# Kernel optimization log

Measured on AMD Instinct MI355X. Metric: run time of the kernel, lower is better.

Reference implementation:

```python
import jax, jax.numpy as jnp
import numpy as np

B, T, O = 8, 8, 25
C, H, W = 3, 192, 640
P = 16            # pooled output size / patch size
D = 768           # embed dim
GH, GW = 12, 2    # max adaptive sampling grid: ceil(H/P), ceil(2*r_max/P)


def setup_inputs() -> dict:
    key = jax.random.key(0)
    k1, k2, k3, k4, k5, k6 = jax.random.split(key, 6)
    features = jax.random.normal(k1, (B, C, T, H, W), jnp.float32)
    # keypoints (x, y, r); x >= H so that the source's buggy y2=min(x+r,H) still yields valid boxes
    kx = jax.random.uniform(k2, (B, T, O), minval=float(H), maxval=float(W))
    ky = jax.random.uniform(k3, (B, T, O), minval=0.0, maxval=float(H))
    kr = jax.random.uniform(k4, (B, T, O), minval=4.0, maxval=16.0)
    keypoints = jnp.stack([kx, ky, kr], axis=-1)
    conv_w = jax.random.normal(k5, (D, C, P, P), jnp.float32) * (1.0 / np.sqrt(C * P * P))
    conv_b = jax.random.normal(k6, (D,), jnp.float32) * 0.01
    return {"features": features, "keypoints": keypoints, "conv_w": conv_w, "conv_b": conv_b}


def _sample_coords(start, bin_sz, grid, G, size):
    # start,bin_sz,grid: [N]; returns coords y/x [N,P,G], validity mask, low idx, high idx, lerp weight
    N = start.shape[0]
    pb = jnp.arange(P, dtype=start.dtype)
    ig = jnp.arange(G, dtype=start.dtype)
    gf = jnp.maximum(grid, 1).astype(start.dtype)
    c = (start[:, None, None]
         + pb[None, :, None] * bin_sz[:, None, None]
         + (ig[None, None, :] + 0.5) * (bin_sz / gf)[:, None, None])  # [N,P,G]
    valid = (jnp.arange(G)[None, None, :] < grid[:, None, None]) & (c >= -1.0) & (c <= float(size))
    cc = jnp.clip(c, 0.0, float(size - 1))
    lo = jnp.floor(cc).astype(jnp.int32)
    hi = jnp.minimum(lo + 1, size - 1)
    l = cc - lo.astype(cc.dtype)  # fractional part (ly/lx)
    return valid, lo, hi, l


def _roi_align(feats_hw, boxes, img_idx):
    # feats_hw: [BT,H,W,C]; boxes: [N,4] xyxy; torchvision roi_align, aligned=True, sampling_ratio=-1
    x1, y1, x2, y2 = boxes[:, 0], boxes[:, 1], boxes[:, 2], boxes[:, 3]
    start_h, start_w = y1 - 0.5, x1 - 0.5  # aligned offset (spatial_scale=1)
    roi_h, roi_w = y2 - y1, x2 - x1        # aligned=True: no clamp to >=1
    bin_h, bin_w = roi_h / P, roi_w / P
    gh = jnp.ceil(roi_h / P).astype(jnp.int32)
    gw = jnp.ceil(roi_w / P).astype(jnp.int32)
    count = jnp.maximum(gh * gw, 1).astype(feats_hw.dtype)

    vy, y0, y1i, ly = _sample_coords(start_h, bin_h, gh, GH, H)  # [N,P,GH]
    vx, x0, x1i, lx = _sample_coords(start_w, bin_w, gw, GW, W)  # [N,P,GW]
    hy, hx = 1.0 - ly, 1.0 - lx

    def gather(yi, xi):  # -> [N,Ph,Pw,GH,GW,C]
        return feats_hw[img_idx[:, None, None, None, None],
                        yi[:, :, None, :, None],
                        xi[:, None, :, None, :]]

    w00 = hy[:, :, None, :, None] * hx[:, None, :, None, :]
    w01 = hy[:, :, None, :, None] * lx[:, None, :, None, :]
    w10 = ly[:, :, None, :, None] * hx[:, None, :, None, :]
    w11 = ly[:, :, None, :, None] * lx[:, None, :, None, :]
    val = (w00[..., None] * gather(y0, x0) + w01[..., None] * gather(y0, x1i)
           + w10[..., None] * gather(y1i, x0) + w11[..., None] * gather(y1i, x1i))
    mask = (vy[:, :, None, :, None] & vx[:, None, :, None, :])[..., None]
    val = jnp.where(mask, val, 0.0)
    return val.sum(axis=(3, 4)) / count[:, None, None, None]  # [N,P,P,C]


def _forward(features, keypoints, conv_w, conv_b):
    feats_hw = features.transpose(0, 2, 3, 4, 1).reshape(B * T, H, W, C)  # (b t) h w c
    kpts = keypoints.reshape(B * T * O, 3)
    kx, ky, kr = kpts[:, 0], kpts[:, 1], kpts[:, 2]
    # faithful to source (note: y2 uses x, a bug in the original module)
    bx1 = jnp.maximum(kx - kr, 0.0)
    by1 = jnp.maximum(ky - kr, 0.0)
    bx2 = jnp.minimum(kx + kr, float(W))
    by2 = jnp.minimum(kx + kr, float(H))
    boxes = jnp.stack([bx1, by1, bx2, by2], axis=-1)
    img_idx = jnp.arange(B * T * O, dtype=jnp.int32) // O
    pooled = _roi_align(feats_hw, boxes, img_idx)  # [N,P,P,C]
    # PxP conv with no padding on PxP input == flatten + linear
    out = jnp.einsum('nijc,dcij->nd', pooled, conv_w) + conv_b
    return out.reshape(B, T, O, D)


def reference(features, keypoints, conv_w, conv_b):
    return _forward(features, keypoints, conv_w, conv_b)
```

## Files before the change

### kernel.cpp

```cpp
#include <hip/hip_runtime.h>

#define NB 8
#define NT 8
#define NO 25
#define NC 3
#define NH 192
#define NW 640
#define NP 16
#define ND 768
#define NGH 12
#define NGW 2
#define NKP (NB*NT*NO)
#define NK (NC*NP*NP)
#define NTASK (NKP*NC)
#define NCVW ((NK*ND)/(256*4))

#define S_STRIDE 41

typedef __attribute__((ext_vector_type(4))) float  f32x4;
typedef __attribute__((ext_vector_type(8))) short  bf16x8;

static __device__ __forceinline__ unsigned short f2bf(float f) {
  union { float f; unsigned u; } x; x.f = f;
  unsigned r = x.u + 0x7FFFu + ((x.u >> 16) & 1u);
  return (unsigned short)(r >> 16);
}

__global__ __launch_bounds__(256) void pool_convw_kernel(
    const float* __restrict__ features,
    const float* __restrict__ keypoints,
    const float* __restrict__ conv_w,
    unsigned short* __restrict__ pooled,
    unsigned short* __restrict__ wbf)
{
  __shared__ float S[NH * S_STRIDE];

  const int bid = blockIdx.x;
  const int tid = threadIdx.x;

  if (bid < NCVW) {
    const int i = bid * 256 + tid;
    const float4 v = reinterpret_cast<const float4*>(conv_w)[i];
    ushort4 o;
    o.x = f2bf(v.x); o.y = f2bf(v.y); o.z = f2bf(v.z); o.w = f2bf(v.w);
    reinterpret_cast<ushort4*>(wbf)[i] = o;
    return;
  }

  const int rb = bid - NCVW;
  const int t  = (rb & 7) * (NTASK / 8) + (rb >> 3);
  const int n  = t / 3;
  const int ch = t - 3 * n;

  const float kx = keypoints[n * 3 + 0];
  const float ky = keypoints[n * 3 + 1];
  const float kr = keypoints[n * 3 + 2];

  const float bx1 = fmaxf(kx - kr, 0.0f);
  const float by1 = fmaxf(ky - kr, 0.0f);
  const float bx2 = fminf(kx + kr, (float)NW);
  const float by2 = fminf(kx + kr, (float)NH);

  const float start_h = by1 - 0.5f;
  const float start_w = bx1 - 0.5f;
  const float bin_h = (by2 - by1) * (1.0f / (float)NP);
  const float bin_w = (bx2 - bx1) * (1.0f / (float)NP);
  const int gh = (int)ceilf(bin_h);
  const int gw = (int)ceilf(bin_w);
  const float ghf = (float)max(gh, 1);
  const float gwf = (float)max(gw, 1);
  const float inv_count = 1.0f / (float)max(gh * gw, 1);
  const float sub_h = bin_h / ghf;
  const float sub_w = bin_w / gwf;

  const float cy_min = start_h + 0.5f * sub_h;
  const float cy_max = start_h + 15.0f * bin_h + ((float)(gh - 1) + 0.5f) * sub_h;
  const float cx_min = start_w + 0.5f * sub_w;
  const float cx_max = start_w + 15.0f * bin_w + ((float)(gw - 1) + 0.5f) * sub_w;
  const int rmin = (int)floorf(fminf(fmaxf(cy_min, 0.0f), (float)(NH - 1)));
  const int rmax = min((int)floorf(fminf(fmaxf(cy_max, 0.0f), (float)(NH - 1))) + 1, NH - 1);
  const int cmin = (int)floorf(fminf(fmaxf(cx_min, 0.0f), (float)(NW - 1)));
  const int cmax = min((int)floorf(fminf(fmaxf(cx_max, 0.0f), (float)(NW - 1))) + 1, NW - 1);
  const int nrows = rmax - rmin + 1;
  const int cmin_al = cmin & ~3;
  const int nq = ((cmax - cmin_al) >> 2) + 1;
  const int tot = nrows * nq;
  const float inv_nq = 1.0f / (float)nq;

  const int img  = n / NO;
  const int bb   = img / NT;
  const int timg = img % NT;
  const float* __restrict__ src =
      features + (size_t)((bb * NC + ch) * NT + timg) * (NH * NW);

  float4 v0, v1, v2, v3, v4, v5, v6, v7;
  int ro0, ro1, ro2, ro3, ro4, ro5, ro6, ro7;

#define STAGE_LOAD(Q, V, RO)                                                 \
  {                                                                          \
    const int e = tid + (Q << 8);                                            \
    if (e < tot) {                                                           \
      const int r  = (int)(((float)e + 0.5f) * inv_nq);                      \
      const int c4 = (e - r * nq) << 2;                                      \
      const int gc = cmin_al + c4;                                           \
      const float* p = src + (size_t)(rmin + r) * NW + gc;                   \
      if (gc + 3 < NW) { V = *reinterpret_cast<const float4*>(p); }          \
      else { V.x = p[0]; V.y = p[min(1, NW - 1 - gc)];                       \
             V.z = p[min(2, NW - 1 - gc)]; V.w = p[min(3, NW - 1 - gc)]; }   \
      RO = r * S_STRIDE + c4;                                                \
    } else { RO = -1; }                                                      \
  }

  STAGE_LOAD(0, v0, ro0) STAGE_LOAD(1, v1, ro1) STAGE_LOAD(2, v2, ro2)
  STAGE_LOAD(3, v3, ro3) STAGE_LOAD(4, v4, ro4) STAGE_LOAD(5, v5, ro5)
  STAGE_LOAD(6, v6, ro6) STAGE_LOAD(7, v7, ro7)
#undef STAGE_LOAD

#define STAGE_WRITE(V, RO)                                                   \
  if (RO >= 0) { float* s = &S[RO];                                          \
    s[0] = V.x; s[1] = V.y; s[2] = V.z; s[3] = V.w; }

  STAGE_WRITE(v0, ro0) STAGE_WRITE(v1, ro1) STAGE_WRITE(v2, ro2)
  STAGE_WRITE(v3, ro3) STAGE_WRITE(v4, ro4) STAGE_WRITE(v5, ro5)
  STAGE_WRITE(v6, ro6) STAGE_WRITE(v7, ro7)
#undef STAGE_WRITE

  const int padc = nq << 2;
  if (tid < nrows) S[tid * S_STRIDE + padc] = 0.0f;

  __syncthreads();

  const int i = tid >> 4;
  const int j = tid & 15;

  float lxv[NGW]; int cxv[NGW];
#pragma unroll
  for (int gx = 0; gx < NGW; ++gx) {
    const float c = start_w + (float)j * bin_w + ((float)gx + 0.5f) * sub_w;
    const float cc = fminf(fmaxf(c, 0.0f), (float)(NW - 1));
    const int x0 = (int)floorf(cc);
    lxv[gx] = cc - (float)x0;
    cxv[gx] = x0 - cmin_al;
  }

  float acc = 0.0f;
#pragma unroll
  for (int gy = 0; gy < NGH; ++gy) {
    if (gy >= gh) break;
    const float c = start_h + (float)i * bin_h + ((float)gy + 0.5f) * sub_h;
    const float cc = fminf(fmaxf(c, 0.0f), (float)(NH - 1));
    const int y0 = (int)floorf(cc);
    const float ly = cc - (float)y0;
    const float hy = 1.0f - ly;
    const int ry0 = (y0 - rmin) * S_STRIDE;
    const int ry1 = (min(y0 + 1, NH - 1) - rmin) * S_STRIDE;
#pragma unroll
    for (int gx = 0; gx < NGW; ++gx) {
      if (gx >= gw) break;
      const float lx = lxv[gx];
      const float hx = 1.0f - lx;
      const float* r0 = &S[ry0 + cxv[gx]];
      const float* r1 = &S[ry1 + cxv[gx]];
      const float v00 = r0[0], v01 = r0[1];
      const float v10 = r1[0], v11 = r1[1];
      acc += hy * (hx * v00 + lx * v01) + ly * (hx * v10 + lx * v11);
    }
  }
  pooled[(size_t)n * NK + ch * (NP * NP) + tid] = f2bf(acc * inv_count);
}

#define BM 64
#define BN 64
#define BK 64

static __device__ __forceinline__ void gld_lds16(const unsigned short* g,
                                                 unsigned short* l) {
  __builtin_amdgcn_global_load_lds(
      (const __attribute__((address_space(1))) unsigned int*)g,
      (__attribute__((address_space(3))) unsigned int*)l,
      16, 0, 0);
}

__global__ __launch_bounds__(256) void gemm_kernel(
    const unsigned short* __restrict__ A,
    const unsigned short* __restrict__ Bw,
    const float* __restrict__ bias,
    float* __restrict__ outp)
{
  __shared__ __align__(16) unsigned short As[2][BM * BK];
  __shared__ __align__(16) unsigned short Bs[2][BM * BK];

  const int tid = threadIdx.x;
  const int w = tid >> 6;
  const int l = tid & 63;
  const int bm = blockIdx.x * BM;
  const int bn = blockIdx.y * BN;

  const int wr = w >> 1, wc = w & 1;
  const int lr = l & 15;
  const int kh = l >> 4;

  const int rA0 = (wr << 5) + lr;
  const int rB0 = (wc << 5) + lr;

#define STAGE(buf, kk)                                                       \
  {                                                                          \
    _Pragma("unroll")                                                        \
    for (int q = 0; q < 2; ++q) {                                            \
      const int s   = (q << 8) + tid;                                        \
      const int row = s >> 3;                                                \
      const int c16 = (s & 7) ^ (row & 7);                                   \
      gld_lds16(A  + (size_t)(bm + row) * NK + (kk) + (c16 << 3),            \
                &As[buf][s << 3]);                                           \
      gld_lds16(Bw + (size_t)(bn + row) * NK + (kk) + (c16 << 3),            \
                &Bs[buf][s << 3]);                                           \
    }                                                                        \
  }

  f32x4 acc[2][2] = {};

  STAGE(0, 0)
  __syncthreads();

  int cur = 0;
  for (int it = 0; it < NK / BK; ++it) {
    if (it + 1 < NK / BK) STAGE(cur ^ 1, (it + 1) * BK)

#pragma unroll
    for (int ks = 0; ks < 2; ++ks) {
      const int kq = (ks << 2) + kh;
      const bf16x8 a0 = *reinterpret_cast<const bf16x8*>(
          &As[cur][(rA0 << 6) + ((kq ^ (rA0 & 7)) << 3)]);
      const bf16x8 a1 = *reinterpret_cast<const bf16x8*>(
          &As[cur][((rA0 + 16) << 6) + ((kq ^ (rA0 & 7)) << 3)]);
      const bf16x8 b0 = *reinterpret_cast<const bf16x8*>(
          &Bs[cur][(rB0 << 6) + ((kq ^ (rB0 & 7)) << 3)]);
      const bf16x8 b1 = *reinterpret_cast<const bf16x8*>(
          &Bs[cur][((rB0 + 16) << 6) + ((kq ^ (rB0 & 7)) << 3)]);
      acc[0][0] = __builtin_amdgcn_mfma_f32_16x16x32_bf16(a0, b0, acc[0][0], 0, 0, 0);
      acc[0][1] = __builtin_amdgcn_mfma_f32_16x16x32_bf16(a0, b1, acc[0][1], 0, 0, 0);
      acc[1][0] = __builtin_amdgcn_mfma_f32_16x16x32_bf16(a1, b0, acc[1][0], 0, 0, 0);
      acc[1][1] = __builtin_amdgcn_mfma_f32_16x16x32_bf16(a1, b1, acc[1][1], 0, 0, 0);
    }

    __syncthreads();
    cur ^= 1;
  }
#undef STAGE

#pragma unroll
  for (int ni = 0; ni < 2; ++ni) {
    const int col = bn + (wc << 5) + (ni << 4) + lr;
    const float bv = bias[col];
#pragma unroll
    for (int mi = 0; mi < 2; ++mi) {
      const int rbase = bm + (wr << 5) + (mi << 4) + (kh << 2);
#pragma unroll
      for (int q = 0; q < 4; ++q) {
        outp[(size_t)(rbase + q) * ND + col] = acc[mi][ni][q] + bv;
      }
    }
  }
}

extern "C" void kernel_launch(void* const* d_in, const int* in_sizes, int n_in,
                              void* d_out, int out_size, void* d_ws, size_t ws_size,
                              hipStream_t stream) {
  (void)in_sizes; (void)n_in; (void)out_size; (void)ws_size;
  const float* features  = (const float*)d_in[0];
  const float* keypoints = (const float*)d_in[1];
  const float* conv_w    = (const float*)d_in[2];
  const float* conv_b    = (const float*)d_in[3];
  float* outp = (float*)d_out;

  unsigned short* pooled = (unsigned short*)d_ws;
  unsigned short* wbf    = (unsigned short*)((char*)d_ws + 2457600);

  pool_convw_kernel<<<NCVW + NTASK, 256, 0, stream>>>(features, keypoints,
                                                      conv_w, pooled, wbf);

  dim3 grid(NKP / BM, ND / BN);
  gemm_kernel<<<grid, 256, 0, stream>>>(pooled, wbf, conv_b, outp);
}
```

Measured before the change: 38.48 us.

## Make pooling kernel persistent with register-prefetched next ROI task

Replaces one-block-per-(ROI,channel) pooling with a fixed grid of 672 persistent blocks, each looping over tasks assigned per XCD. While one task is computed from LDS, the next task's global loads are issued into registers, so load latency overlaps with compute. The conv weight bf16 conversion is spread across the same blocks instead of using separate blocks. This cuts block launch overhead and hides memory latency, at the cost of an extra sync per task, higher register pressure and possible load imbalance across blocks.

```diff
diff --git a/kernel.cpp b/kernel.cpp
--- a/kernel.cpp
+++ b/kernel.cpp
@@ -13,9 +13,14 @@
 #define NKP (NB*NT*NO)
 #define NK (NC*NP*NP)
 #define NTASK (NKP*NC)
-#define NCVW ((NK*ND)/(256*4))
 
 #define S_STRIDE 41
+
+#define POOL_BLOCKS 672
+#define TASKS_PER_XCD 600
+#define BLOCKS_PER_XCD 84
+#define CVW_TOTAL ((NK*ND)/4)
+#define CVW_PER_BLOCK 220
 
 typedef __attribute__((ext_vector_type(4))) float  f32x4;
 typedef __attribute__((ext_vector_type(8))) short  bf16x8;
@@ -26,7 +31,58 @@
   return (unsigned short)(r >> 16);
 }
 
-__global__ __launch_bounds__(256) void pool_convw_kernel(
+struct TaskGeom {
+  const float* src;
+  float start_h, start_w, bin_h, bin_w, sub_h, sub_w, inv_count, inv_nq;
+  int n, ch, gh, gw, rmin, cmin_al, nq, nrows, tot;
+};
+
+static __device__ __forceinline__ TaskGeom make_geom(
+    const float* __restrict__ features, const float* __restrict__ keypoints,
+    int t) {
+  TaskGeom G;
+  G.n  = t / 3;
+  G.ch = t - 3 * G.n;
+  const float kx = keypoints[G.n * 3 + 0];
+  const float ky = keypoints[G.n * 3 + 1];
+  const float kr = keypoints[G.n * 3 + 2];
+  const float bx1 = fmaxf(kx - kr, 0.0f);
+  const float by1 = fmaxf(ky - kr, 0.0f);
+  const float bx2 = fminf(kx + kr, (float)NW);
+  const float by2 = fminf(kx + kr, (float)NH);
+  G.start_h = by1 - 0.5f;
+  G.start_w = bx1 - 0.5f;
+  G.bin_h = (by2 - by1) * (1.0f / (float)NP);
+  G.bin_w = (bx2 - bx1) * (1.0f / (float)NP);
+  G.gh = (int)ceilf(G.bin_h);
+  G.gw = (int)ceilf(G.bin_w);
+  const float ghf = (float)max(G.gh, 1);
+  const float gwf = (float)max(G.gw, 1);
+  G.inv_count = 1.0f / (float)max(G.gh * G.gw, 1);
+  G.sub_h = G.bin_h / ghf;
+  G.sub_w = G.bin_w / gwf;
+  const float cy_min = G.start_h + 0.5f * G.sub_h;
+  const float cy_max = G.start_h + 15.0f * G.bin_h + ((float)(G.gh - 1) + 0.5f) * G.sub_h;
+  const float cx_min = G.start_w + 0.5f * G.sub_w;
+  const float cx_max = G.start_w + 15.0f * G.bin_w + ((float)(G.gw - 1) + 0.5f) * G.sub_w;
+  G.rmin = (int)floorf(fminf(fmaxf(cy_min, 0.0f), (float)(NH - 1)));
+  const int rmax = min((int)floorf(fminf(fmaxf(cy_max, 0.0f), (float)(NH - 1))) + 1, NH - 1);
+  const int cmin = (int)floorf(fminf(fmaxf(cx_min, 0.0f), (float)(NW - 1)));
+  const int cmax = min((int)floorf(fminf(fmaxf(cx_max, 0.0f), (float)(NW - 1))) + 1, NW - 1);
+  G.nrows = rmax - G.rmin + 1;
+  G.cmin_al = cmin & ~3;
+  G.nq = ((cmax - G.cmin_al) >> 2) + 1;
+  G.tot = G.nrows * G.nq;
+  G.inv_nq = 1.0f / (float)G.nq;
+  const int img  = G.n / NO;
+  const int bb   = img / NT;
+  const int timg = img - bb * NT;
+  G.src = features + (size_t)((bb * NC + G.ch) * NT + timg) * (NH * NW)
+        + (size_t)G.rmin * NW;
+  return G;
+}
+
+__global__ __launch_bounds__(256) void pool_kernel(
     const float* __restrict__ features,
     const float* __restrict__ keypoints,
     const float* __restrict__ conv_w,
@@ -35,138 +91,116 @@
 {
   __shared__ float S[NH * S_STRIDE];
 
-  const int bid = blockIdx.x;
+  const int p   = blockIdx.x;
   const int tid = threadIdx.x;
 
-  if (bid < NCVW) {
-    const int i = bid * 256 + tid;
-    const float4 v = reinterpret_cast<const float4*>(conv_w)[i];
-    ushort4 o;
-    o.x = f2bf(v.x); o.y = f2bf(v.y); o.z = f2bf(v.z); o.w = f2bf(v.w);
-    reinterpret_cast<ushort4*>(wbf)[i] = o;
-    return;
-  }
-
-  const int rb = bid - NCVW;
-  const int t  = (rb & 7) * (NTASK / 8) + (rb >> 3);
-  const int n  = t / 3;
-  const int ch = t - 3 * n;
-
-  const float kx = keypoints[n * 3 + 0];
-  const float ky = keypoints[n * 3 + 1];
-  const float kr = keypoints[n * 3 + 2];
-
-  const float bx1 = fmaxf(kx - kr, 0.0f);
-  const float by1 = fmaxf(ky - kr, 0.0f);
-  const float bx2 = fminf(kx + kr, (float)NW);
-  const float by2 = fminf(kx + kr, (float)NH);
-
-  const float start_h = by1 - 0.5f;
-  const float start_w = bx1 - 0.5f;
-  const float bin_h = (by2 - by1) * (1.0f / (float)NP);
-  const float bin_w = (bx2 - bx1) * (1.0f / (float)NP);
-  const int gh = (int)ceilf(bin_h);
-  const int gw = (int)ceilf(bin_w);
-  const float ghf = (float)max(gh, 1);
-  const float gwf = (float)max(gw, 1);
-  const float inv_count = 1.0f / (float)max(gh * gw, 1);
-  const float sub_h = bin_h / ghf;
-  const float sub_w = bin_w / gwf;
-
-  const float cy_min = start_h + 0.5f * sub_h;
-  const float cy_max = start_h + 15.0f * bin_h + ((float)(gh - 1) + 0.5f) * sub_h;
-  const float cx_min = start_w + 0.5f * sub_w;
-  const float cx_max = start_w + 15.0f * bin_w + ((float)(gw - 1) + 0.5f) * sub_w;
-  const int rmin = (int)floorf(fminf(fmaxf(cy_min, 0.0f), (float)(NH - 1)));
-  const int rmax = min((int)floorf(fminf(fmaxf(cy_max, 0.0f), (float)(NH - 1))) + 1, NH - 1);
-  const int cmin = (int)floorf(fminf(fmaxf(cx_min, 0.0f), (float)(NW - 1)));
-  const int cmax = min((int)floorf(fminf(fmaxf(cx_max, 0.0f), (float)(NW - 1))) + 1, NW - 1);
-  const int nrows = rmax - rmin + 1;
-  const int cmin_al = cmin & ~3;
-  const int nq = ((cmax - cmin_al) >> 2) + 1;
-  const int tot = nrows * nq;
-  const float inv_nq = 1.0f / (float)nq;
-
-  const int img  = n / NO;
-  const int bb   = img / NT;
-  const int timg = img % NT;
-  const float* __restrict__ src =
-      features + (size_t)((bb * NC + ch) * NT + timg) * (NH * NW);
+  const int widx = p * CVW_PER_BLOCK + tid;
+  const bool wact = (tid < CVW_PER_BLOCK) && (widx < CVW_TOTAL);
+  float4 wv = {};
+  if (wact) wv = reinterpret_cast<const float4*>(conv_w)[widx];
+
+  const int xcd = p & 7;
+  const int lb  = p >> 3;
+  const int tbase = xcd * TASKS_PER_XCD + lb;
+  const int ntasks = (TASKS_PER_XCD - lb + BLOCKS_PER_XCD - 1) / BLOCKS_PER_XCD;
+
+  TaskGeom gc = make_geom(features, keypoints, tbase);
 
   float4 v0, v1, v2, v3, v4, v5, v6, v7;
   int ro0, ro1, ro2, ro3, ro4, ro5, ro6, ro7;
 
-#define STAGE_LOAD(Q, V, RO)                                                 \
+#define STAGE_LOAD(G, Q, V, RO)                                              \
   {                                                                          \
     const int e = tid + (Q << 8);                                            \
-    if (e < tot) {                                                           \
-      const int r  = (int)(((float)e + 0.5f) * inv_nq);                      \
-      const int c4 = (e - r * nq) << 2;                                      \
-      const int gc = cmin_al + c4;                                           \
-      const float* p = src + (size_t)(rmin + r) * NW + gc;                   \
-      if (gc + 3 < NW) { V = *reinterpret_cast<const float4*>(p); }          \
-      else { V.x = p[0]; V.y = p[min(1, NW - 1 - gc)];                       \
-             V.z = p[min(2, NW - 1 - gc)]; V.w = p[min(3, NW - 1 - gc)]; }   \
+    if (e < G.tot) {                                                         \
+      const int r  = (int)(((float)e + 0.5f) * G.inv_nq);                    \
+      const int c4 = (e - r * G.nq) << 2;                                    \
+      const int gcl = G.cmin_al + c4;                                        \
+      const float* pp = G.src + (size_t)r * NW + gcl;                        \
+      if (gcl + 3 < NW) { V = *reinterpret_cast<const float4*>(pp); }        \
+      else { V.x = pp[0]; V.y = pp[min(1, NW - 1 - gcl)];                    \
+             V.z = pp[min(2, NW - 1 - gcl)]; V.w = pp[min(3, NW - 1 - gcl)]; } \
       RO = r * S_STRIDE + c4;                                                \
     } else { RO = -1; }                                                      \
   }
-
-  STAGE_LOAD(0, v0, ro0) STAGE_LOAD(1, v1, ro1) STAGE_LOAD(2, v2, ro2)
-  STAGE_LOAD(3, v3, ro3) STAGE_LOAD(4, v4, ro4) STAGE_LOAD(5, v5, ro5)
-  STAGE_LOAD(6, v6, ro6) STAGE_LOAD(7, v7, ro7)
-#undef STAGE_LOAD
+#define STAGE_ALL(G)                                                         \
+  STAGE_LOAD(G, 0, v0, ro0) STAGE_LOAD(G, 1, v1, ro1)                        \
+  STAGE_LOAD(G, 2, v2, ro2) STAGE_LOAD(G, 3, v3, ro3)                        \
+  STAGE_LOAD(G, 4, v4, ro4) STAGE_LOAD(G, 5, v5, ro5)                        \
+  STAGE_LOAD(G, 6, v6, ro6) STAGE_LOAD(G, 7, v7, ro7)
 
 #define STAGE_WRITE(V, RO)                                                   \
   if (RO >= 0) { float* s = &S[RO];                                          \
     s[0] = V.x; s[1] = V.y; s[2] = V.z; s[3] = V.w; }
-
-  STAGE_WRITE(v0, ro0) STAGE_WRITE(v1, ro1) STAGE_WRITE(v2, ro2)
-  STAGE_WRITE(v3, ro3) STAGE_WRITE(v4, ro4) STAGE_WRITE(v5, ro5)
+#define STAGE_WRITE_ALL()                                                    \
+  STAGE_WRITE(v0, ro0) STAGE_WRITE(v1, ro1) STAGE_WRITE(v2, ro2)             \
+  STAGE_WRITE(v3, ro3) STAGE_WRITE(v4, ro4) STAGE_WRITE(v5, ro5)             \
   STAGE_WRITE(v6, ro6) STAGE_WRITE(v7, ro7)
-#undef STAGE_WRITE
-
-  const int padc = nq << 2;
-  if (tid < nrows) S[tid * S_STRIDE + padc] = 0.0f;
-
-  __syncthreads();
+
+  STAGE_ALL(gc)
+
+  if (wact) {
+    ushort4 o;
+    o.x = f2bf(wv.x); o.y = f2bf(wv.y); o.z = f2bf(wv.z); o.w = f2bf(wv.w);
+    reinterpret_cast<ushort4*>(wbf)[widx] = o;
+  }
 
   const int i = tid >> 4;
   const int j = tid & 15;
 
-  float lxv[NGW]; int cxv[NGW];
-#pragma unroll
-  for (int gx = 0; gx < NGW; ++gx) {
-    const float c = start_w + (float)j * bin_w + ((float)gx + 0.5f) * sub_w;
-    const float cc = fminf(fmaxf(c, 0.0f), (float)(NW - 1));
-    const int x0 = (int)floorf(cc);
-    lxv[gx] = cc - (float)x0;
-    cxv[gx] = x0 - cmin_al;
-  }
-
-  float acc = 0.0f;
-#pragma unroll
-  for (int gy = 0; gy < NGH; ++gy) {
-    if (gy >= gh) break;
-    const float c = start_h + (float)i * bin_h + ((float)gy + 0.5f) * sub_h;
-    const float cc = fminf(fmaxf(c, 0.0f), (float)(NH - 1));
-    const int y0 = (int)floorf(cc);
-    const float ly = cc - (float)y0;
-    const float hy = 1.0f - ly;
-    const int ry0 = (y0 - rmin) * S_STRIDE;
-    const int ry1 = (min(y0 + 1, NH - 1) - rmin) * S_STRIDE;
+  for (int k = 0; k < ntasks; ++k) {
+    const bool more = (k + 1 < ntasks);
+    TaskGeom gn;
+    if (more) gn = make_geom(features, keypoints, tbase + (k + 1) * BLOCKS_PER_XCD);
+
+    STAGE_WRITE_ALL()
+    if (tid < gc.nrows) S[tid * S_STRIDE + (gc.nq << 2)] = 0.0f;
+    __syncthreads();
+
+    if (more) { STAGE_ALL(gn) }
+
+    float lxv[NGW]; int cxv[NGW];
 #pragma unroll
     for (int gx = 0; gx < NGW; ++gx) {
-      if (gx >= gw) break;
-      const float lx = lxv[gx];
-      const float hx = 1.0f - lx;
-      const float* r0 = &S[ry0 + cxv[gx]];
-      const float* r1 = &S[ry1 + cxv[gx]];
-      const float v00 = r0[0], v01 = r0[1];
-      const float v10 = r1[0], v11 = r1[1];
-      acc += hy * (hx * v00 + lx * v01) + ly * (hx * v10 + lx * v11);
+      const float c = gc.start_w + (float)j * gc.bin_w + ((float)gx + 0.5f) * gc.sub_w;
+      const float cc = fminf(fmaxf(c, 0.0f), (float)(NW - 1));
+      const int x0 = (int)floorf(cc);
+      lxv[gx] = cc - (float)x0;
+      cxv[gx] = x0 - gc.cmin_al;
     }
-  }
-  pooled[(size_t)n * NK + ch * (NP * NP) + tid] = f2bf(acc * inv_count);
+
+    float acc = 0.0f;
+#pragma unroll
+    for (int gy = 0; gy < NGH; ++gy) {
+      if (gy >= gc.gh) break;
+      const float c = gc.start_h + (float)i * gc.bin_h + ((float)gy + 0.5f) * gc.sub_h;
+      const float cc = fminf(fmaxf(c, 0.0f), (float)(NH - 1));
+      const int y0 = (int)floorf(cc);
+      const float ly = cc - (float)y0;
+      const float hy = 1.0f - ly;
+      const int ry0 = (y0 - gc.rmin) * S_STRIDE;
+      const int ry1 = (min(y0 + 1, NH - 1) - gc.rmin) * S_STRIDE;
+#pragma unroll
+      for (int gx = 0; gx < NGW; ++gx) {
+        if (gx >= gc.gw) break;
+        const float lx = lxv[gx];
+        const float hx = 1.0f - lx;
+        const float* r0 = &S[ry0 + cxv[gx]];
+        const float* r1 = &S[ry1 + cxv[gx]];
+        const float s00 = r0[0], s01 = r0[1];
+        const float s10 = r1[0], s11 = r1[1];
+        acc += hy * (hx * s00 + lx * s01) + ly * (hx * s10 + lx * s11);
+      }
+    }
+    pooled[(size_t)gc.n * NK + gc.ch * (NP * NP) + tid] = f2bf(acc * gc.inv_count);
+
+    __syncthreads();
+    if (more) gc = gn;
+  }
+#undef STAGE_ALL
+#undef STAGE_LOAD
+#undef STAGE_WRITE
+#undef STAGE_WRITE_ALL
 }
 
 #define BM 64
@@ -276,8 +310,8 @@
   unsigned short* pooled = (unsigned short*)d_ws;
   unsigned short* wbf    = (unsigned short*)((char*)d_ws + 2457600);
 
-  pool_convw_kernel<<<NCVW + NTASK, 256, 0, stream>>>(features, keypoints,
-                                                      conv_w, pooled, wbf);
+  pool_kernel<<<POOL_BLOCKS, 256, 0, stream>>>(features, keypoints, conv_w,
+                                               pooled, wbf);
 
   dim3 grid(NKP / BM, ND / BN);
   gemm_kernel<<<grid, 256, 0, stream>>>(pooled, wbf, conv_b, outp);
```

Result: slower. 56.01 us (+45.6%).
